# Kernel optimization log

Measured on AMD Instinct MI355X. Metric: run time of the kernel, lower is better.

## Reference

```python
import jax, jax.numpy as jnp
import numpy as np

D = 512
V = 1024


def setup_inputs() -> dict:
    key = jax.random.key(0)
    k1, k2, k3, k4 = jax.random.split(key, 4)
    enc = jax.random.normal(k1, (8, 256, D), dtype=jnp.float32)
    dec = jax.random.normal(k2, (8, 64, D), dtype=jnp.float32)
    # nn.Linear(input_size, vocab_size): weight (V, D), bias (V), uniform(-1/sqrt(D), 1/sqrt(D))
    bound = 1.0 / np.sqrt(D)
    W = jax.random.uniform(k3, (V, D), dtype=jnp.float32, minval=-bound, maxval=bound)
    b = jax.random.uniform(k4, (V,), dtype=jnp.float32, minval=-bound, maxval=bound)
    return {"encoder_outputs": enc, "decoder_outputs": dec, "W": W, "b": b}


def reference(encoder_outputs, decoder_outputs, W, b):
    # (B,T,1,D) + (B,1,U,D) -> (B,T,U,D), then Linear to (B,T,U,V)
    joint = encoder_outputs[:, :, None, :] + decoder_outputs[:, None, :, :]
    return jnp.einsum('btud,vd->btuv', joint, W) + b
```

## Files before the change

kernel.cpp:

```cpp
#include <hip/hip_runtime.h>
#include <cstddef>

#define GEMM_K 512
#define GEMM_N 1024

typedef __attribute__((ext_vector_type(4))) float f4;

__global__ __launch_bounds__(256) void gemm_joint(
    const float* __restrict__ enc,
    const float* __restrict__ dec,
    const float* __restrict__ W,
    const float* __restrict__ bias,
    float* __restrict__ EC)
{
    __shared__ float As[64 * 32];
    __shared__ float Ws[128 * 32];

    const int tid = threadIdx.x;
    const int m0 = blockIdx.x * 64;
    const int n0 = blockIdx.y * 128;
    const bool is_enc = (m0 < 2048);
    const float* __restrict__ Abase =
        is_enc ? (enc + (size_t)m0 * GEMM_K) : (dec + (size_t)(m0 - 2048) * GEMM_K);

    const int tx = tid & 15;
    const int ty = tid >> 4;

    float acc[4][8];
#pragma unroll
    for (int i = 0; i < 4; ++i)
#pragma unroll
        for (int j = 0; j < 8; ++j) acc[i][j] = 0.f;

    const int ar = tid >> 3;
    const int ak = tid & 7;

    float4 ra[2], rw[4];
    {
        const float* ap = Abase + (size_t)ar * GEMM_K + (ak << 2);
        ra[0] = *(const float4*)(ap);
        ra[1] = *(const float4*)(ap + 32 * GEMM_K);
        const float* wp = W + (size_t)(n0 + ar) * GEMM_K + (ak << 2);
        rw[0] = *(const float4*)(wp);
        rw[1] = *(const float4*)(wp + 32 * GEMM_K);
        rw[2] = *(const float4*)(wp + 64 * GEMM_K);
        rw[3] = *(const float4*)(wp + 96 * GEMM_K);
    }

    for (int k0 = 0; k0 < GEMM_K; k0 += 32) {
        {
            const int r0 = ar, r1 = ar + 32;
            const int q0 = (ak ^ (r0 >> 3)) & 7;
            const int q1 = (ak ^ (r1 >> 3)) & 7;
            *(float4*)(&As[r0 * 32 + q0 * 4]) = ra[0];
            *(float4*)(&As[r1 * 32 + q1 * 4]) = ra[1];
#pragma unroll
            for (int i = 0; i < 4; ++i) {
                const int r = ar + 32 * i;
                const int q = (ak ^ (r >> 3)) & 7;
                *(float4*)(&Ws[r * 32 + q * 4]) = rw[i];
            }
        }
        __syncthreads();

        if (k0 + 32 < GEMM_K) {
            const float* ap = Abase + (size_t)ar * GEMM_K + (k0 + 32) + (ak << 2);
            ra[0] = *(const float4*)(ap);
            ra[1] = *(const float4*)(ap + 32 * GEMM_K);
            const float* wp = W + (size_t)(n0 + ar) * GEMM_K + (k0 + 32) + (ak << 2);
            rw[0] = *(const float4*)(wp);
            rw[1] = *(const float4*)(wp + 32 * GEMM_K);
            rw[2] = *(const float4*)(wp + 64 * GEMM_K);
            rw[3] = *(const float4*)(wp + 96 * GEMM_K);
        }

#pragma unroll
        for (int kq = 0; kq < 8; ++kq) {
            f4 a4[4], b4[8];
            const int pb = ((kq ^ tx) & 7) << 2;
#pragma unroll
            for (int i = 0; i < 4; ++i) {
                const int m = ty * 4 + i;
                a4[i] = *(const f4*)(&As[m * 32 + (((kq ^ (m >> 3)) & 7) << 2)]);
            }
#pragma unroll
            for (int j = 0; j < 8; ++j) {
                b4[j] = *(const f4*)(&Ws[(tx * 8 + j) * 32 + pb]);
            }
#pragma unroll
            for (int i = 0; i < 4; ++i)
#pragma unroll
                for (int j = 0; j < 8; ++j) {
                    acc[i][j] = fmaf(a4[i].x, b4[j].x, acc[i][j]);
                    acc[i][j] = fmaf(a4[i].y, b4[j].y, acc[i][j]);
                    acc[i][j] = fmaf(a4[i].z, b4[j].z, acc[i][j]);
                    acc[i][j] = fmaf(a4[i].w, b4[j].w, acc[i][j]);
                }
        }
        __syncthreads();
    }

    float4 bia = make_float4(0.f, 0.f, 0.f, 0.f);
    float4 bib = make_float4(0.f, 0.f, 0.f, 0.f);
    if (is_enc) {
        bia = *(const float4*)(bias + n0 + tx * 8);
        bib = *(const float4*)(bias + n0 + tx * 8 + 4);
    }
#pragma unroll
    for (int i = 0; i < 4; ++i) {
        const int m = m0 + ty * 4 + i;
        float4 c0 = make_float4(acc[i][0] + bia.x, acc[i][1] + bia.y,
                                acc[i][2] + bia.z, acc[i][3] + bia.w);
        float4 c1 = make_float4(acc[i][4] + bib.x, acc[i][5] + bib.y,
                                acc[i][6] + bib.z, acc[i][7] + bib.w);
        float* crow = EC + (size_t)m * GEMM_N + n0 + tx * 8;
        *(float4*)(crow) = c0;
        *(float4*)(crow + 4) = c1;
    }
}

__global__ __launch_bounds__(256) void bcast_add(
    const float* __restrict__ EC, float* __restrict__ out)
{
    const int bt = blockIdx.x;
    const int b = bt >> 8;
    const int tid = threadIdx.x;

    const f4 e = ((const f4*)(EC + (size_t)bt * 1024))[tid];
    const f4* __restrict__ dbase = (const f4*)(EC + (size_t)(2048 + b * 64) * 1024);
    f4* __restrict__ obase = (f4*)(out + (size_t)bt * 64 * 1024);

#pragma unroll 8
    for (int u = 0; u < 64; ++u) {
        f4 d = dbase[u * 256 + tid];
        obase[u * 256 + tid] = e + d;
    }
}

extern "C" void kernel_launch(void* const* d_in, const int* in_sizes, int n_in,
                              void* d_out, int out_size, void* d_ws, size_t ws_size,
                              hipStream_t stream) {
    const float* enc  = (const float*)d_in[0];
    const float* dec  = (const float*)d_in[1];
    const float* W    = (const float*)d_in[2];
    const float* bias = (const float*)d_in[3];
    float* out = (float*)d_out;
    float* EC = (float*)d_ws;

    dim3 g1(40, 8);
    gemm_joint<<<g1, dim3(256), 0, stream>>>(enc, dec, W, bias, EC);
    bcast_add<<<2048, 256, 0, stream>>>(EC, out);
}
```

Baseline: 645.2 us.

## Fuse GEMM and broadcast-add into one kernel staging E and D tiles in LDS

Merges the two launches into one kernel. Each 512-thread block computes a 64-row encoder tile and its batch's 64-row decoder tile against a 128-column slice of W. The results go to shared memory, then the block writes the full 64x64x128 broadcast sum directly to the output. This removes the workspace round-trip for the intermediate products and the second launch. The cost is that the decoder GEMM is recomputed once per encoder tile (four times per batch), and only 256 blocks are launched, which may leave CUs underfilled during the store-bound phase.

```diff
diff --git a/kernel.cpp b/kernel.cpp
--- a/kernel.cpp
+++ b/kernel.cpp
@@ -1,30 +1,37 @@
 #include <hip/hip_runtime.h>
 #include <cstddef>
 
-#define GEMM_K 512
-#define GEMM_N 1024
-
 typedef __attribute__((ext_vector_type(4))) float f4;
 
-__global__ __launch_bounds__(256) void gemm_joint(
+#define GK 512
+#define GN 1024
+
+__global__ __launch_bounds__(512) void joint_fused(
     const float* __restrict__ enc,
     const float* __restrict__ dec,
     const float* __restrict__ W,
     const float* __restrict__ bias,
-    float* __restrict__ EC)
+    float* __restrict__ out)
 {
-    __shared__ float As[64 * 32];
-    __shared__ float Ws[128 * 32];
+    __shared__ float smem[16384];
+    float* As = smem;
+    float* Ws = smem + 4096;
+    float* Es = smem;
+    float* Ds = smem + 8192;
 
     const int tid = threadIdx.x;
-    const int m0 = blockIdx.x * 64;
-    const int n0 = blockIdx.y * 128;
-    const bool is_enc = (m0 < 2048);
-    const float* __restrict__ Abase =
-        is_enc ? (enc + (size_t)m0 * GEMM_K) : (dec + (size_t)(m0 - 2048) * GEMM_K);
+    const int bt0 = blockIdx.x * 64;
+    const int b   = blockIdx.x >> 2;
+    const int v0  = blockIdx.y * 128;
+
+    const float* __restrict__ Ae = enc + (size_t)bt0 * GK;
+    const float* __restrict__ Ad = dec + (size_t)b * 64 * GK;
+    const float* __restrict__ Wv = W + (size_t)v0 * GK;
 
     const int tx = tid & 15;
     const int ty = tid >> 4;
+    const int ar = tid >> 3;
+    const int ak = tid & 7;
 
     float acc[4][8];
 #pragma unroll
@@ -32,46 +39,35 @@
 #pragma unroll
         for (int j = 0; j < 8; ++j) acc[i][j] = 0.f;
 
-    const int ar = tid >> 3;
-    const int ak = tid & 7;
-
-    float4 ra[2], rw[4];
+    f4 rae, rad, rw0, rw1;
     {
-        const float* ap = Abase + (size_t)ar * GEMM_K + (ak << 2);
-        ra[0] = *(const float4*)(ap);
-        ra[1] = *(const float4*)(ap + 32 * GEMM_K);
-        const float* wp = W + (size_t)(n0 + ar) * GEMM_K + (ak << 2);
-        rw[0] = *(const float4*)(wp);
-        rw[1] = *(const float4*)(wp + 32 * GEMM_K);
-        rw[2] = *(const float4*)(wp + 64 * GEMM_K);
-        rw[3] = *(const float4*)(wp + 96 * GEMM_K);
+        const float* pe = Ae + (size_t)ar * GK + (ak << 2);
+        const float* pd = Ad + (size_t)ar * GK + (ak << 2);
+        const float* pw = Wv + (size_t)ar * GK + (ak << 2);
+        rae = *(const f4*)pe;
+        rad = *(const f4*)pd;
+        rw0 = *(const f4*)pw;
+        rw1 = *(const f4*)(pw + (size_t)64 * GK);
     }
 
-    for (int k0 = 0; k0 < GEMM_K; k0 += 32) {
+    for (int k0 = 0; k0 < GK; k0 += 32) {
         {
-            const int r0 = ar, r1 = ar + 32;
-            const int q0 = (ak ^ (r0 >> 3)) & 7;
-            const int q1 = (ak ^ (r1 >> 3)) & 7;
-            *(float4*)(&As[r0 * 32 + q0 * 4]) = ra[0];
-            *(float4*)(&As[r1 * 32 + q1 * 4]) = ra[1];
-#pragma unroll
-            for (int i = 0; i < 4; ++i) {
-                const int r = ar + 32 * i;
-                const int q = (ak ^ (r >> 3)) & 7;
-                *(float4*)(&Ws[r * 32 + q * 4]) = rw[i];
-            }
+            const int q = ((ak ^ (ar >> 3)) & 7) << 2;
+            *(f4*)(&As[ar * 32 + q])         = rae;
+            *(f4*)(&As[(64 + ar) * 32 + q])  = rad;
+            *(f4*)(&Ws[ar * 32 + q])         = rw0;
+            *(f4*)(&Ws[(64 + ar) * 32 + q])  = rw1;
         }
         __syncthreads();
 
-        if (k0 + 32 < GEMM_K) {
-            const float* ap = Abase + (size_t)ar * GEMM_K + (k0 + 32) + (ak << 2);
-            ra[0] = *(const float4*)(ap);
-            ra[1] = *(const float4*)(ap + 32 * GEMM_K);
-            const float* wp = W + (size_t)(n0 + ar) * GEMM_K + (k0 + 32) + (ak << 2);
-            rw[0] = *(const float4*)(wp);
-            rw[1] = *(const float4*)(wp + 32 * GEMM_K);
-            rw[2] = *(const float4*)(wp + 64 * GEMM_K);
-            rw[3] = *(const float4*)(wp + 96 * GEMM_K);
+        if (k0 + 32 < GK) {
+            const float* pe = Ae + (size_t)ar * GK + (k0 + 32) + (ak << 2);
+            const float* pd = Ad + (size_t)ar * GK + (k0 + 32) + (ak << 2);
+            const float* pw = Wv + (size_t)ar * GK + (k0 + 32) + (ak << 2);
+            rae = *(const f4*)pe;
+            rad = *(const f4*)pd;
+            rw0 = *(const f4*)pw;
+            rw1 = *(const f4*)(pw + (size_t)64 * GK);
         }
 
 #pragma unroll
@@ -100,40 +96,45 @@
         __syncthreads();
     }
 
-    float4 bia = make_float4(0.f, 0.f, 0.f, 0.f);
-    float4 bib = make_float4(0.f, 0.f, 0.f, 0.f);
-    if (is_enc) {
-        bia = *(const float4*)(bias + n0 + tx * 8);
-        bib = *(const float4*)(bias + n0 + tx * 8 + 4);
+    {
+        const bool isE = (ty < 16);
+        f4 bi0 = {0.f, 0.f, 0.f, 0.f}, bi1 = {0.f, 0.f, 0.f, 0.f};
+        if (isE) {
+            bi0 = *(const f4*)(bias + v0 + tx * 8);
+            bi1 = *(const f4*)(bias + v0 + tx * 8 + 4);
+        }
+        float* Cs = isE ? Es : Ds;
+        const int mloc = (ty & 15) * 4;
+#pragma unroll
+        for (int i = 0; i < 4; ++i) {
+            f4 c0 = {acc[i][0] + bi0.x, acc[i][1] + bi0.y,
+                     acc[i][2] + bi0.z, acc[i][3] + bi0.w};
+            f4 c1 = {acc[i][4] + bi1.x, acc[i][5] + bi1.y,
+                     acc[i][6] + bi1.z, acc[i][7] + bi1.w};
+            *(f4*)(&Cs[(mloc + i) * 128 + tx * 8])     = c0;
+            *(f4*)(&Cs[(mloc + i) * 128 + tx * 8 + 4]) = c1;
+        }
     }
+    __syncthreads();
+
+    {
+        const int v4 = tid & 31;
+        const int rlane = tid >> 5;
+        const f4* Es4 = (const f4*)Es;
+        const f4* Ds4 = (const f4*)Ds;
+        float* obase = out + (size_t)bt0 * 64 * GN + v0 + 4 * v4;
+
+#pragma unroll 2
+        for (int g = 0; g < 64; ++g) {
+            const f4 e4 = Es4[g * 32 + v4];
+            float* orow = obase + (size_t)g * 64 * GN;
 #pragma unroll
-    for (int i = 0; i < 4; ++i) {
-        const int m = m0 + ty * 4 + i;
-        float4 c0 = make_float4(acc[i][0] + bia.x, acc[i][1] + bia.y,
-                                acc[i][2] + bia.z, acc[i][3] + bia.w);
-        float4 c1 = make_float4(acc[i][4] + bib.x, acc[i][5] + bib.y,
-                                acc[i][6] + bib.z, acc[i][7] + bib.w);
-        float* crow = EC + (size_t)m * GEMM_N + n0 + tx * 8;
-        *(float4*)(crow) = c0;
-        *(float4*)(crow + 4) = c1;
-    }
-}
-
-__global__ __launch_bounds__(256) void bcast_add(
-    const float* __restrict__ EC, float* __restrict__ out)
-{
-    const int bt = blockIdx.x;
-    const int b = bt >> 8;
-    const int tid = threadIdx.x;
-
-    const f4 e = ((const f4*)(EC + (size_t)bt * 1024))[tid];
-    const f4* __restrict__ dbase = (const f4*)(EC + (size_t)(2048 + b * 64) * 1024);
-    f4* __restrict__ obase = (f4*)(out + (size_t)bt * 64 * 1024);
-
-#pragma unroll 8
-    for (int u = 0; u < 64; ++u) {
-        f4 d = dbase[u * 256 + tid];
-        obase[u * 256 + tid] = e + d;
+            for (int s = 0; s < 4; ++s) {
+                const int u = s * 16 + rlane;
+                const f4 d4 = Ds4[u * 32 + v4];
+                *(f4*)(orow + (size_t)u * GN) = e4 + d4;
+            }
+        }
     }
 }
 
@@ -145,9 +146,8 @@
     const float* W    = (const float*)d_in[2];
     const float* bias = (const float*)d_in[3];
     float* out = (float*)d_out;
-    float* EC = (float*)d_ws;
 
-    dim3 g1(40, 8);
-    gemm_joint<<<g1, dim3(256), 0, stream>>>(enc, dec, W, bias, EC);
-    bcast_add<<<2048, 256, 0, stream>>>(EC, out);
+    (void)d_ws; (void)ws_size;
+
+    joint_fused<<<dim3(32, 8), dim3(512), 0, stream>>>(enc, dec, W, bias, out);
 }
```

After: 594.4 us. -7.9%, faster.
